# Kernel optimization log

Hardware: AMD Instinct MI355X
Metric: run time of the kernel (lower is better)

## Reference

```python
import jax, jax.numpy as jnp
import numpy as np

B, S, H, DH, DE, DC = 32, 1024, 2, 64, 128, 64  # batch, seq, heads, dim_head, dim_emb, dim_ctx


def setup_inputs() -> dict:
    key = jax.random.key(0)
    ks = jax.random.split(key, 16)
    p = lambda k, shp: (jax.random.normal(k, shp, dtype=jnp.float32) * 0.02)
    return {
        "queries_it": jax.random.normal(ks[0], (B, S, DE), dtype=jnp.float32),
        "queries_ctx": jax.random.normal(ks[1], (B, S, DC), dtype=jnp.float32),
        "keys_it": jax.random.normal(ks[2], (B, S, DE), dtype=jnp.float32),
        "keys_ctx": jax.random.normal(ks[3], (B, S, DC), dtype=jnp.float32),
        "sigma_noise": jax.random.uniform(ks[4], (B, H), dtype=jnp.float32),
        "noise": jax.random.normal(ks[5], (B, 2, S, S), dtype=jnp.float32),
        "Wq_it": p(ks[6], (DH, DE)), "bq_it": jnp.zeros((DH,), jnp.float32),
        "Wk_it": p(ks[7], (DH, DE)), "bk_it": jnp.zeros((DH,), jnp.float32),
        "Wq_ctx": p(ks[8], (DH, DC)), "bq_ctx": jnp.zeros((DH,), jnp.float32),
        "Wk_ctx": p(ks[9], (DH, DC)), "bk_ctx": jnp.zeros((DH,), jnp.float32),
        "Wv": p(ks[10], (DE, DE)), "bv": jnp.zeros((DE,), jnp.float32),
        "W1": p(ks[11], (H, 2)), "b1": jnp.zeros((H,), jnp.float32),
        "W2": p(ks[12], (H, H)), "b2": jnp.zeros((H,), jnp.float32),
    }


def reference(queries_it, queries_ctx, keys_it, keys_ctx, sigma_noise, noise,
              Wq_it, bq_it, Wk_it, bk_it, Wq_ctx, bq_ctx, Wk_ctx, bk_ctx,
              Wv, bv, W1, b1, W2, b2):
    # dual QK projections
    Q_it = queries_it @ Wq_it.T + bq_it          # [B,Sq,DH]
    K_it = keys_it @ Wk_it.T + bk_it             # [B,Sk,DH]
    Q_ctx = queries_ctx @ Wq_ctx.T + bq_ctx
    K_ctx = keys_ctx @ Wk_ctx.T + bk_ctx
    s_it = jnp.einsum('bqd,bkd->bqk', Q_it, K_it)
    s_ctx = jnp.einsum('bqd,bkd->bqk', Q_ctx, K_ctx)
    scores = jnp.stack([s_it, s_ctx], axis=1)    # [B,2,Sq,Sk]
    # additive per-head noise (sigma viewed [B,H,1,1], H==2)
    scores = scores + noise * (sigma_noise[:, :, None, None] ** 2)
    # per-element HDP MLP: 2 -> H -> H over last axis
    x = jnp.transpose(scores, (0, 2, 3, 1))      # [B,Sq,Sk,2]
    h = jax.nn.relu(x @ W1.T + b1)
    s = h @ W2.T + b2                            # [B,Sq,Sk,H]
    s = jnp.transpose(s, (0, 3, 1, 2)) / (DH ** 0.5)  # [B,H,Sq,Sk]
    # key padding mask
    key_mask = jnp.sign(jnp.sum(jnp.abs(keys_it), axis=-1))      # [B,Sk]
    s = jnp.where(key_mask[:, None, None, :] == 0, -1e9, s)
    att = jax.nn.softmax(s, axis=-1)
    # query padding mask (applied after softmax, as in the original)
    query_mask = jnp.sign(jnp.sum(jnp.abs(queries_it), axis=-1))  # [B,Sq]
    att = att * query_mask[:, None, :, None]
    # values
    V = (keys_it @ Wv.T + bv).reshape(B, S, H, DH)               # [B,Sk,H,DH]
    out = jnp.einsum('bhqk,bkhd->bqhd', att, V).reshape(B, S, H * DH)
    return out + queries_it
```

## Files before the change

kernel.cpp:

```cpp
#include <hip/hip_runtime.h>

#define B_N 32
#define S_N 1024

typedef __attribute__((ext_vector_type(8))) short sh8;
typedef __attribute__((ext_vector_type(4))) short sh4;
typedef __attribute__((ext_vector_type(4))) float f4;

#define AS1 __attribute__((address_space(1)))
#define AS3 __attribute__((address_space(3)))

__device__ __forceinline__ short f2bf(float f) {
  unsigned u = __builtin_bit_cast(unsigned, f);
  u += 0x7fff + ((u >> 16) & 1);
  return (short)(u >> 16);
}

#if defined(__has_builtin)
#if __has_builtin(__builtin_amdgcn_mfma_f32_16x16x16bf16_1k)
#define HAVE_MFMA16 1
#endif
#endif
__device__ __forceinline__ f4 mfma16(sh4 a, sh4 b, f4 c) {
#ifdef HAVE_MFMA16
  return __builtin_amdgcn_mfma_f32_16x16x16bf16_1k(a, b, c, 0, 0, 0);
#else
  asm volatile("v_mfma_f32_16x16x16_bf16 %0, %1, %2, %0\n\ts_nop 7\n\ts_nop 7"
               : "+v"(c) : "v"(a), "v"(b));
  return c;
#endif
}

__device__ __forceinline__ sh8 cvt8(const float* src, float& s) {
  f4 x0 = *(const f4*)src;
  f4 x1 = *(const f4*)(src + 4);
  sh8 v;
#pragma unroll
  for (int i = 0; i < 4; ++i) {
    v[i] = f2bf(x0[i]);
    v[4 + i] = f2bf(x1[i]);
    s += fabsf(x0[i]) + fabsf(x1[i]);
  }
  return v;
}

template <int DIN, bool MASK>
__global__ __launch_bounds__(256) void proj_mfma(
    const float* __restrict__ in, const float* __restrict__ W,
    const float* __restrict__ bias, short* __restrict__ out,
    float* __restrict__ mask) {
  constexpr int NSL = DIN / 8;
  constexpr int KT = DIN / 32;
  __shared__ __align__(16) short a_t[128 * DIN];
  __shared__ __align__(16) short w_t[64 * DIN];
  const int tid = threadIdx.x;
  const int wave = tid >> 6, lane = tid & 63;
  const int col = lane & 15, grp = lane >> 4;
  const size_t r0g = (size_t)blockIdx.x * 128;

#pragma unroll
  for (int t = 0; t < 128 * NSL / 256; ++t) {
    const int u = t * 256 + tid, row = u / NSL, sl = u % NSL;
    float s = 0.f;
    sh8 v = cvt8(in + (r0g + row) * DIN + sl * 8, s);
    *(sh8*)&a_t[(row * NSL + (sl ^ (row & (NSL - 1)))) * 8] = v;
    if (MASK) {
      s += __shfl_xor(s, 1); s += __shfl_xor(s, 2);
      s += __shfl_xor(s, 4); s += __shfl_xor(s, 8);
      if ((lane & 15) == 0) mask[r0g + row] = (s != 0.f) ? 1.f : 0.f;
    }
  }
#pragma unroll
  for (int t = 0; t < 64 * NSL / 256; ++t) {
    const int u = t * 256 + tid, row = u / NSL, sl = u % NSL;
    float s = 0.f;
    sh8 v = cvt8(W + (size_t)row * DIN + sl * 8, s);
    *(sh8*)&w_t[(row * NSL + (sl ^ (row & (NSL - 1)))) * 8] = v;
  }
  __syncthreads();

  const int r0 = wave * 32;
  sh8 a[2][KT];
#pragma unroll
  for (int ri = 0; ri < 2; ++ri)
#pragma unroll
    for (int t = 0; t < KT; ++t) {
      const int row = r0 + ri * 16 + col;
      a[ri][t] = *(const sh8*)&a_t[(row * NSL + ((grp + 4 * t) ^ (row & (NSL - 1)))) * 8];
    }
  f4 acc[2][4];
#pragma unroll
  for (int ri = 0; ri < 2; ++ri)
#pragma unroll
    for (int jt = 0; jt < 4; ++jt) acc[ri][jt] = (f4)0.f;
#pragma unroll
  for (int jt = 0; jt < 4; ++jt) {
    const int j = jt * 16 + col;
    sh8 bw[KT];
#pragma unroll
    for (int t = 0; t < KT; ++t)
      bw[t] = *(const sh8*)&w_t[(j * NSL + ((grp + 4 * t) ^ (j & (NSL - 1)))) * 8];
#pragma unroll
    for (int ri = 0; ri < 2; ++ri)
#pragma unroll
      for (int t = 0; t < KT; ++t)
        acc[ri][jt] = __builtin_amdgcn_mfma_f32_16x16x32_bf16(a[ri][t], bw[t], acc[ri][jt], 0, 0, 0);
  }
#pragma unroll
  for (int jt = 0; jt < 4; ++jt) {
    const float bj = bias[jt * 16 + col];
#pragma unroll
    for (int ri = 0; ri < 2; ++ri)
#pragma unroll
      for (int r = 0; r < 4; ++r)
        out[(r0g + r0 + ri * 16 + grp * 4 + r) * 64 + jt * 16 + col] = f2bf(acc[ri][jt][r] + bj);
  }
}

__global__ __launch_bounds__(256) void proj_k_mfma(
    const float* __restrict__ in, const float* __restrict__ Wk, const float* __restrict__ bk_,
    const float* __restrict__ Wv, const float* __restrict__ bv_,
    short* __restrict__ kit, short* __restrict__ vt, float* __restrict__ km) {
  __shared__ __align__(16) char ulds[65536];
  short* a_t = (short*)ulds;
  short* w_t = (short*)(ulds + 32768);
  const int tid = threadIdx.x;
  const int wave = tid >> 6, lane = tid & 63;
  const int col = lane & 15, grp = lane >> 4;
  const size_t r0g = (size_t)blockIdx.x * 128;
  const int bb = (int)(r0g >> 10), s0 = (int)(r0g & 1023);

#pragma unroll
  for (int t = 0; t < 8; ++t) {
    const int u = t * 256 + tid, row = u >> 4, sl = u & 15;
    float s = 0.f;
    sh8 v = cvt8(in + (r0g + row) * 128 + sl * 8, s);
    *(sh8*)&a_t[(row * 16 + (sl ^ (row & 15))) * 8] = v;
    s += __shfl_xor(s, 1); s += __shfl_xor(s, 2);
    s += __shfl_xor(s, 4); s += __shfl_xor(s, 8);
    if ((lane & 15) == 0) km[r0g + row] = (s != 0.f) ? 1.f : 0.f;
  }
#pragma unroll
  for (int t = 0; t < 8; ++t) {
    const int u = t * 256 + tid, row = u >> 4, sl = u & 15;
    const float* src = (row < 64) ? (Wk + (size_t)row * 128) : (Wv + (size_t)(row - 64) * 128);
    float s = 0.f;
    sh8 v = cvt8(src + sl * 8, s);
    *(sh8*)&w_t[(row * 16 + (sl ^ (row & 15))) * 8] = v;
  }
  __syncthreads();

  const int r0 = wave * 32;
  sh8 a[2][4];
#pragma unroll
  for (int ri = 0; ri < 2; ++ri)
#pragma unroll
    for (int t = 0; t < 4; ++t) {
      const int row = r0 + ri * 16 + col;
      a[ri][t] = *(const sh8*)&a_t[(row * 16 + ((grp + 4 * t) ^ (row & 15))) * 8];
    }
  f4 acck[2][4], accv[2][8];
#pragma unroll
  for (int ri = 0; ri < 2; ++ri) {
#pragma unroll
    for (int jt = 0; jt < 4; ++jt) acck[ri][jt] = (f4)0.f;
#pragma unroll
    for (int jt = 0; jt < 8; ++jt) accv[ri][jt] = (f4)0.f;
  }
#pragma unroll
  for (int jt = 0; jt < 8; ++jt) {
    const int j = jt * 16 + col;
    sh8 bw[4];
#pragma unroll
    for (int t = 0; t < 4; ++t)
      bw[t] = *(const sh8*)&w_t[(j * 16 + ((grp + 4 * t) ^ (j & 15))) * 8];
#pragma unroll
    for (int ri = 0; ri < 2; ++ri)
#pragma unroll
      for (int t = 0; t < 4; ++t) {
        f4& dst = (jt < 4) ? acck[ri][jt] : accv[ri][jt - 4];
        dst = __builtin_amdgcn_mfma_f32_16x16x32_bf16(a[ri][t], bw[t], dst, 0, 0, 0);
      }
  }
#pragma unroll
  for (int jt = 0; jt < 4; ++jt) {
    const float bj = bk_[jt * 16 + col];
#pragma unroll
    for (int ri = 0; ri < 2; ++ri)
#pragma unroll
      for (int r = 0; r < 4; ++r)
        kit[(r0g + r0 + ri * 16 + grp * 4 + r) * 64 + jt * 16 + col] = f2bf(acck[ri][jt][r] + bj);
  }
  __syncthreads();
#pragma unroll
  for (int t = 0; t < 4; ++t) {
    const int u = t * 256 + tid, row = u >> 4, sl = u & 15;
    float s = 0.f;
    sh8 v = cvt8(Wv + (size_t)(64 + row) * 128 + sl * 8, s);
    *(sh8*)&w_t[(row * 16 + (sl ^ (row & 15))) * 8] = v;
  }
  __syncthreads();
#pragma unroll
  for (int jt = 0; jt < 4; ++jt) {
    const int j = jt * 16 + col;
    sh8 bw[4];
#pragma unroll
    for (int t = 0; t < 4; ++t)
      bw[t] = *(const sh8*)&w_t[(j * 16 + ((grp + 4 * t) ^ (j & 15))) * 8];
#pragma unroll
    for (int ri = 0; ri < 2; ++ri)
#pragma unroll
      for (int t = 0; t < 4; ++t)
        accv[ri][4 + jt] = __builtin_amdgcn_mfma_f32_16x16x32_bf16(a[ri][t], bw[t], accv[ri][4 + jt], 0, 0, 0);
  }
  __syncthreads();
  short* vtile = (short*)ulds;
#pragma unroll
  for (int vjt = 0; vjt < 8; ++vjt) {
    const int j = vjt * 16 + col;
    const float bvj = bv_[j];
#pragma unroll
    for (int ri = 0; ri < 2; ++ri)
#pragma unroll
      for (int r = 0; r < 4; ++r)
        vtile[j * 136 + r0 + ri * 16 + grp * 4 + r] = f2bf(accv[ri][vjt][r] + bvj);
  }
  __syncthreads();
  const int j2 = tid >> 1, half = tid & 1;
  short* dst = vt + ((size_t)(bb * 128 + j2)) * S_N + s0 + half * 64;
#pragma unroll
  for (int i = 0; i < 8; ++i)
    *(sh8*)(dst + i * 8) = *(const sh8*)&vtile[j2 * 136 + half * 64 + i * 8];
}

__global__ __launch_bounds__(256, 2) void attn_kernel(
    const short* __restrict__ qit, const short* __restrict__ kit,
    const short* __restrict__ qctx, const short* __restrict__ kctx,
    const short* __restrict__ vt,
    const float* __restrict__ noise,
    const float* __restrict__ sigma,
    const float* __restrict__ qmask, const float* __restrict__ kmask,
    const float* __restrict__ qin,
    const float* __restrict__ W1, const float* __restrict__ b1,
    const float* __restrict__ W2, const float* __restrict__ b2,
    float* __restrict__ out) {
  __shared__ __align__(16) char bufs[4][16384];
  __shared__ float kml[1024];
  __shared__ float lsum_lds[4][2][16];

  const int tid = threadIdx.x;
  const int wave = tid >> 6, lane = tid & 63;
  const int bid = blockIdx.x;
  const int wg = ((bid & 7) << 6) | (bid >> 3);
  const int b = wg >> 4, qt = wg & 15;
  const int qblk = qt * 64;
  const int qbase = qblk + wave * 16;
  const int col = lane & 15, grp = lane >> 4;
  const int swk = col & 7;

  const float w100 = W1[0], w101 = W1[1], w110 = W1[2], w111 = W1[3];
  const float bb10 = b1[0], bb11 = b1[1];
  const float sc = 0.125f;
  const float w200 = W2[0] * sc, w201 = W2[1] * sc, w210 = W2[2] * sc, w211 = W2[3] * sc;
  const float bb20 = b2[0] * sc, bb21 = b2[1] * sc;
  float sg0 = sigma[b * 2 + 0]; sg0 *= sg0;
  float sg1 = sigma[b * 2 + 1]; sg1 *= sg1;

  const int qrow = qbase + col;
  sh8 aqit[2], aqctx[2];
#pragma unroll
  for (int t = 0; t < 2; ++t) {
    aqit[t] = *(const sh8*)(qit + ((size_t)(b * S_N + qrow)) * 64 + grp * 8 + t * 32);
    aqctx[t] = *(const sh8*)(qctx + ((size_t)(b * S_N + qrow)) * 64 + grp * 8 + t * 32);
  }

  f4 acc[2][4];
#pragma unroll
  for (int h = 0; h < 2; ++h)
#pragma unroll
    for (int dt = 0; dt < 4; ++dt) acc[h][dt] = (f4)0.f;
  float rs0 = 0.f, rs1 = 0.f;

  const float* nz_g = noise + (size_t)(b * 2) * S_N * S_N;
  const short* kit_g = kit + (size_t)b * S_N * 64;
  const short* kctx_g = kctx + (size_t)b * S_N * 64;
  const short* vt_g = vt + (size_t)b * 128 * S_N;

  for (int i = tid; i < 1024; i += 256) kml[i] = kmask[(size_t)b * S_N + i];

  auto STAGE = [&](char* buf, int kc) {
    if (wave == 0) {
#pragma unroll
      for (int j = 0; j < 2; ++j) {
        const int u = j * 64 + lane, row = u >> 3, sl = u & 7;
        const size_t off = (size_t)(kc + row) * 64 + ((sl ^ (row & 7)) << 3);
        __builtin_amdgcn_global_load_lds((const AS1 unsigned*)(kit_g + off),
                                         (AS3 unsigned*)(buf + j * 1024), 16, 0, 0);
        __builtin_amdgcn_global_load_lds((const AS1 unsigned*)(kctx_g + off),
                                         (AS3 unsigned*)(buf + 2048 + j * 1024), 16, 0, 0);
      }
    } else if (wave == 1) {
#pragma unroll
      for (int j = 0; j < 4; ++j) {
        const int u = j * 64 + lane, d = u >> 1, sl = u & 1;
        const short* g = vt_g + (size_t)d * S_N + kc + ((sl ^ (d & 1)) << 3);
        __builtin_amdgcn_global_load_lds((const AS1 unsigned*)g,
                                         (AS3 unsigned*)(buf + 4096 + j * 1024), 16, 0, 0);
      }
    } else {
#pragma unroll
      for (int j = 0; j < 4; ++j) {
        const int un = (wave - 2) * 4 + j;
        const int u = un * 64 + lane, r = u >> 2, head = r >> 6, q = r & 63, sl = u & 3;
        const float* g = nz_g + (size_t)head * S_N * S_N + (size_t)(qblk + q) * S_N + kc +
                         ((sl ^ (q & 3)) << 2);
        __builtin_amdgcn_global_load_lds((const AS1 unsigned*)g,
                                         (AS3 unsigned*)(buf + 8192 + un * 1024), 16, 0, 0);
      }
    }
  };

  STAGE(bufs[0], 0);
  STAGE(bufs[1], 16);
  STAGE(bufs[2], 32);

#pragma unroll 1
  for (int k = 0; k < 64; ++k) {
    asm volatile("s_waitcnt vmcnt(8)" ::: "memory");
    __builtin_amdgcn_sched_barrier(0);
    __builtin_amdgcn_s_barrier();
    STAGE(bufs[(k + 3) & 3], ((k + 3) & 63) * 16);

    const char* cur = bufs[k & 3];
    const short* Kb = (const short*)cur;
    const short* Cb = (const short*)(cur + 2048);
    const short* Vb = (const short*)(cur + 4096);
    const float* Nb = (const float*)(cur + 8192);

    f4 sit = (f4)0.f, sctx = (f4)0.f;
#pragma unroll
    for (int t = 0; t < 2; ++t) {
      const int so = ((grp + 4 * t) ^ swk) * 8;
      sh8 bk = *(const sh8*)&Kb[col * 64 + so];
      sit = __builtin_amdgcn_mfma_f32_16x16x32_bf16(bk, aqit[t], sit, 0, 0, 0);
      sh8 bc = *(const sh8*)&Cb[col * 64 + so];
      sctx = __builtin_amdgcn_mfma_f32_16x16x32_bf16(bc, aqctx[t], sctx, 0, 0, 0);
    }
    const int qrl = wave * 16 + col;
    const int nso = (grp ^ (col & 3)) << 2;
    f4 n0 = *(const f4*)&Nb[qrl * 16 + nso];
    f4 n1 = *(const f4*)&Nb[(64 + qrl) * 16 + nso];
    f4 km = *(const f4*)&kml[k * 16 + grp * 4];
    sh4 po, pc;
#pragma unroll
    for (int r = 0; r < 4; ++r) {
      float x0 = fmaf(n0[r], sg0, sit[r]);
      float x1 = fmaf(n1[r], sg1, sctx[r]);
      float h0 = fmaxf(fmaf(w101, x1, fmaf(w100, x0, bb10)), 0.f);
      float h1 = fmaxf(fmaf(w111, x1, fmaf(w110, x0, bb11)), 0.f);
      float L0 = fmaf(w201, h1, fmaf(w200, h0, bb20));
      float L1 = fmaf(w211, h1, fmaf(w210, h0, bb21));
      float p0 = __expf(L0) * km[r];
      float p1 = __expf(L1) * km[r];
      rs0 += p0;
      rs1 += p1;
      po[r] = f2bf(p0);
      pc[r] = f2bf(p1);
    }
#pragma unroll
    for (int h = 0; h < 2; ++h) {
      const sh4 pa = h ? pc : po;
#pragma unroll
      for (int dt = 0; dt < 4; ++dt) {
        const int drow = h * 64 + dt * 16 + col;
        const int phys = (grp >> 1) ^ (drow & 1);
        sh4 bv = *(const sh4*)&Vb[drow * 16 + phys * 8 + (grp & 1) * 4];
        acc[h][dt] = mfma16(pa, bv, acc[h][dt]);
      }
    }
  }

  rs0 += __shfl_xor(rs0, 16); rs0 += __shfl_xor(rs0, 32);
  rs1 += __shfl_xor(rs1, 16); rs1 += __shfl_xor(rs1, 32);
  if (lane < 16) {
    lsum_lds[wave][0][col] = rs0;
    lsum_lds[wave][1][col] = rs1;
  }
  __syncthreads();
  f4 ls0 = *(const f4*)&lsum_lds[wave][0][grp * 4];
  f4 ls1 = *(const f4*)&lsum_lds[wave][1][grp * 4];
  f4 qm4 = *(const f4*)(qmask + (size_t)b * S_N + qbase + grp * 4);
#pragma unroll
  for (int h = 0; h < 2; ++h)
#pragma unroll
    for (int dt = 0; dt < 4; ++dt)
#pragma unroll
      for (int r = 0; r < 4; ++r) {
        const float s2 = qm4[r] / (h ? ls1[r] : ls0[r]);
        const size_t o = ((size_t)(b * S_N + qbase + grp * 4 + r)) * 128 + h * 64 + dt * 16 + col;
        out[o] = acc[h][dt][r] * s2 + qin[o];
      }
}

extern "C" void kernel_launch(void* const* d_in, const int* in_sizes, int n_in,
                              void* d_out, int out_size, void* d_ws, size_t ws_size,
                              hipStream_t stream) {
  const float* queries_it = (const float*)d_in[0];
  const float* queries_ctx = (const float*)d_in[1];
  const float* keys_it = (const float*)d_in[2];
  const float* keys_ctx = (const float*)d_in[3];
  const float* sigma = (const float*)d_in[4];
  const float* noise = (const float*)d_in[5];
  const float* Wq_it = (const float*)d_in[6];
  const float* bq_it = (const float*)d_in[7];
  const float* Wk_it = (const float*)d_in[8];
  const float* bk_it = (const float*)d_in[9];
  const float* Wq_ctx = (const float*)d_in[10];
  const float* bq_ctx = (const float*)d_in[11];
  const float* Wk_ctx = (const float*)d_in[12];
  const float* bk_ctx = (const float*)d_in[13];
  const float* Wv = (const float*)d_in[14];
  const float* bv = (const float*)d_in[15];
  const float* W1 = (const float*)d_in[16];
  const float* b1 = (const float*)d_in[17];
  const float* W2 = (const float*)d_in[18];
  const float* b2 = (const float*)d_in[19];
  float* out = (float*)d_out;

  char* ws = (char*)d_ws;
  short* qit = (short*)(ws);
  short* kit = (short*)(ws + (4ull << 20));
  short* qctx = (short*)(ws + (8ull << 20));
  short* kctx = (short*)(ws + (12ull << 20));
  short* vt = (short*)(ws + (16ull << 20));
  float* qmask = (float*)(ws + (24ull << 20));
  float* kmask = (float*)(ws + (24ull << 20) + (size_t)B_N * S_N * 4);

  const int NB = B_N * S_N / 128;
  proj_mfma<128, true><<<dim3(NB), 256, 0, stream>>>(queries_it, Wq_it, bq_it, qit, qmask);
  proj_k_mfma<<<dim3(NB), 256, 0, stream>>>(keys_it, Wk_it, bk_it, Wv, bv, kit, vt, kmask);
  proj_mfma<64, false><<<dim3(NB), 256, 0, stream>>>(queries_ctx, Wq_ctx, bq_ctx, qctx, nullptr);
  proj_mfma<64, false><<<dim3(NB), 256, 0, stream>>>(keys_ctx, Wk_ctx, bk_ctx, kctx, nullptr);

  attn_kernel<<<dim3(B_N * (S_N / 64)), 256, 0, stream>>>(
      qit, kit, qctx, kctx, vt, noise, sigma, qmask, kmask, queries_it,
      W1, b1, W2, b2, out);
}
```

Measured before the change: 127.0 us.

## Shrink attention workgroups to 32 queries with 2 waves and triple buffering

The attention kernel now uses 128-thread workgroups that each handle 32 query rows, so twice as many workgroups are launched. The staging pipeline drops from 4 to 3 LDS buffers of 12 KB, and the K/V/noise loads are redistributed across the two waves. The key mask is stored in LDS as bf16 to save space. The aim is lower LDS use per workgroup and higher occupancy, at the cost of loading each K/V tile twice as often per query row and a shallower prefetch depth.

```diff
diff --git a/kernel.cpp b/kernel.cpp
--- a/kernel.cpp
+++ b/kernel.cpp
@@ -14,6 +14,10 @@
   unsigned u = __builtin_bit_cast(unsigned, f);
   u += 0x7fff + ((u >> 16) & 1);
   return (short)(u >> 16);
+}
+__device__ __forceinline__ float bf2f(short s) {
+  unsigned u = ((unsigned)(unsigned short)s) << 16;
+  return __builtin_bit_cast(float, u);
 }
 
 #if defined(__has_builtin)
@@ -233,7 +237,7 @@
     *(sh8*)(dst + i * 8) = *(const sh8*)&vtile[j2 * 136 + half * 64 + i * 8];
 }
 
-__global__ __launch_bounds__(256, 2) void attn_kernel(
+__global__ __launch_bounds__(128, 2) void attn_kernel(
     const short* __restrict__ qit, const short* __restrict__ kit,
     const short* __restrict__ qctx, const short* __restrict__ kctx,
     const short* __restrict__ vt,
@@ -244,16 +248,16 @@
     const float* __restrict__ W1, const float* __restrict__ b1,
     const float* __restrict__ W2, const float* __restrict__ b2,
     float* __restrict__ out) {
-  __shared__ __align__(16) char bufs[4][16384];
-  __shared__ float kml[1024];
-  __shared__ float lsum_lds[4][2][16];
+  __shared__ __align__(16) char bufs[3][12288];
+  __shared__ unsigned short kml[1024];
+  __shared__ float lsum_lds[2][2][16];
 
   const int tid = threadIdx.x;
   const int wave = tid >> 6, lane = tid & 63;
   const int bid = blockIdx.x;
-  const int wg = ((bid & 7) << 6) | (bid >> 3);
-  const int b = wg >> 4, qt = wg & 15;
-  const int qblk = qt * 64;
+  const int wg = ((bid & 7) << 7) | (bid >> 3);
+  const int b = wg >> 5, qt = wg & 31;
+  const int qblk = qt * 32;
   const int qbase = qblk + wave * 16;
   const int col = lane & 15, grp = lane >> 4;
   const int swk = col & 7;
@@ -286,7 +290,8 @@
   const short* kctx_g = kctx + (size_t)b * S_N * 64;
   const short* vt_g = vt + (size_t)b * 128 * S_N;
 
-  for (int i = tid; i < 1024; i += 256) kml[i] = kmask[(size_t)b * S_N + i];
+  for (int i = tid; i < 1024; i += 128)
+    kml[i] = (unsigned short)f2bf(kmask[(size_t)b * S_N + i]);
 
   auto STAGE = [&](char* buf, int kc) {
     if (wave == 0) {
@@ -299,43 +304,52 @@
         __builtin_amdgcn_global_load_lds((const AS1 unsigned*)(kctx_g + off),
                                          (AS3 unsigned*)(buf + 2048 + j * 1024), 16, 0, 0);
       }
-    } else if (wave == 1) {
-#pragma unroll
-      for (int j = 0; j < 4; ++j) {
-        const int u = j * 64 + lane, d = u >> 1, sl = u & 1;
+#pragma unroll
+      for (int un = 0; un < 2; ++un) {
+        const int u = un * 64 + lane, d = u >> 1, sl = u & 1;
         const short* g = vt_g + (size_t)d * S_N + kc + ((sl ^ (d & 1)) << 3);
         __builtin_amdgcn_global_load_lds((const AS1 unsigned*)g,
-                                         (AS3 unsigned*)(buf + 4096 + j * 1024), 16, 0, 0);
+                                         (AS3 unsigned*)(buf + 4096 + un * 1024), 16, 0, 0);
       }
     } else {
 #pragma unroll
+      for (int un = 2; un < 4; ++un) {
+        const int u = un * 64 + lane, d = u >> 1, sl = u & 1;
+        const short* g = vt_g + (size_t)d * S_N + kc + ((sl ^ (d & 1)) << 3);
+        __builtin_amdgcn_global_load_lds((const AS1 unsigned*)g,
+                                         (AS3 unsigned*)(buf + 4096 + un * 1024), 16, 0, 0);
+      }
+#pragma unroll
       for (int j = 0; j < 4; ++j) {
-        const int un = (wave - 2) * 4 + j;
-        const int u = un * 64 + lane, r = u >> 2, head = r >> 6, q = r & 63, sl = u & 3;
+        const int u = j * 64 + lane, r = u >> 2, head = r >> 5, q = r & 31, sl = u & 3;
         const float* g = nz_g + (size_t)head * S_N * S_N + (size_t)(qblk + q) * S_N + kc +
-                         ((sl ^ (q & 3)) << 2);
+                         ((sl ^ (r & 3)) << 2);
         __builtin_amdgcn_global_load_lds((const AS1 unsigned*)g,
-                                         (AS3 unsigned*)(buf + 8192 + un * 1024), 16, 0, 0);
+                                         (AS3 unsigned*)(buf + 8192 + j * 1024), 16, 0, 0);
       }
     }
   };
 
   STAGE(bufs[0], 0);
   STAGE(bufs[1], 16);
-  STAGE(bufs[2], 32);
-
+
+  int cur = 0;
 #pragma unroll 1
   for (int k = 0; k < 64; ++k) {
-    asm volatile("s_waitcnt vmcnt(8)" ::: "memory");
+    asm volatile("s_waitcnt vmcnt(6)" ::: "memory");
     __builtin_amdgcn_sched_barrier(0);
     __builtin_amdgcn_s_barrier();
-    STAGE(bufs[(k + 3) & 3], ((k + 3) & 63) * 16);
-
-    const char* cur = bufs[k & 3];
-    const short* Kb = (const short*)cur;
-    const short* Cb = (const short*)(cur + 2048);
-    const short* Vb = (const short*)(cur + 4096);
-    const float* Nb = (const float*)(cur + 8192);
+    {
+      int nb = cur + 2;
+      if (nb >= 3) nb -= 3;
+      STAGE(bufs[nb], ((k + 2) & 63) * 16);
+    }
+
+    const char* cb = bufs[cur];
+    const short* Kb = (const short*)cb;
+    const short* Cb = (const short*)(cb + 2048);
+    const short* Vb = (const short*)(cb + 4096);
+    const float* Nb = (const float*)(cb + 8192);
 
     f4 sit = (f4)0.f, sctx = (f4)0.f;
 #pragma unroll
@@ -349,8 +363,8 @@
     const int qrl = wave * 16 + col;
     const int nso = (grp ^ (col & 3)) << 2;
     f4 n0 = *(const f4*)&Nb[qrl * 16 + nso];
-    f4 n1 = *(const f4*)&Nb[(64 + qrl) * 16 + nso];
-    f4 km = *(const f4*)&kml[k * 16 + grp * 4];
+    f4 n1 = *(const f4*)&Nb[(32 + qrl) * 16 + nso];
+    sh4 kmv = *(const sh4*)&kml[k * 16 + grp * 4];
     sh4 po, pc;
 #pragma unroll
     for (int r = 0; r < 4; ++r) {
@@ -360,8 +374,9 @@
       float h1 = fmaxf(fmaf(w111, x1, fmaf(w110, x0, bb11)), 0.f);
       float L0 = fmaf(w201, h1, fmaf(w200, h0, bb20));
       float L1 = fmaf(w211, h1, fmaf(w210, h0, bb21));
-      float p0 = __expf(L0) * km[r];
-      float p1 = __expf(L1) * km[r];
+      const float kmf = bf2f(kmv[r]);
+      float p0 = __expf(L0) * kmf;
+      float p1 = __expf(L1) * kmf;
       rs0 += p0;
       rs1 += p1;
       po[r] = f2bf(p0);
@@ -378,6 +393,8 @@
         acc[h][dt] = mfma16(pa, bv, acc[h][dt]);
       }
     }
+    ++cur;
+    if (cur >= 3) cur = 0;
   }
 
   rs0 += __shfl_xor(rs0, 16); rs0 += __shfl_xor(rs0, 32);
@@ -442,7 +459,7 @@
   proj_mfma<64, false><<<dim3(NB), 256, 0, stream>>>(queries_ctx, Wq_ctx, bq_ctx, qctx, nullptr);
   proj_mfma<64, false><<<dim3(NB), 256, 0, stream>>>(keys_ctx, Wk_ctx, bk_ctx, kctx, nullptr);
 
-  attn_kernel<<<dim3(B_N * (S_N / 64)), 256, 0, stream>>>(
+  attn_kernel<<<dim3(B_N * (S_N / 32)), 128, 0, stream>>>(
       qit, kit, qctx, kctx, vt, noise, sigma, qmask, kmask, queries_it,
       W1, b1, W2, b2, out);
 }
```

Result: slower. 151.0 us (+18.9%).

## Rebalance attention staging loads across waves and merge ctx projection launches

Applied to the files above, without the earlier changes.

Each wave now loads its own slice of the noise tile, and the K/ctx/V loads are split evenly across waves instead of one wave carrying the whole noise load. A second, finer vmcnt wait lets the QK MFMAs start before each wave's noise data has landed. The two ctx projection kernels are merged into one launch, cutting launch overhead and the tail between them. A __syncthreads is added after filling the key mask in LDS, which fixes a potential race at a small sync cost.

```diff
diff --git a/kernel.cpp b/kernel.cpp
--- a/kernel.cpp
+++ b/kernel.cpp
@@ -45,10 +45,10 @@
 }
 
 template <int DIN, bool MASK>
-__global__ __launch_bounds__(256) void proj_mfma(
+__device__ __forceinline__ void dev_proj(
     const float* __restrict__ in, const float* __restrict__ W,
     const float* __restrict__ bias, short* __restrict__ out,
-    float* __restrict__ mask) {
+    float* __restrict__ mask, int blk) {
   constexpr int NSL = DIN / 8;
   constexpr int KT = DIN / 32;
   __shared__ __align__(16) short a_t[128 * DIN];
@@ -56,7 +56,7 @@
   const int tid = threadIdx.x;
   const int wave = tid >> 6, lane = tid & 63;
   const int col = lane & 15, grp = lane >> 4;
-  const size_t r0g = (size_t)blockIdx.x * 128;
+  const size_t r0g = (size_t)blk * 128;
 
 #pragma unroll
   for (int t = 0; t < 128 * NSL / 256; ++t) {
@@ -115,6 +115,24 @@
       for (int r = 0; r < 4; ++r)
         out[(r0g + r0 + ri * 16 + grp * 4 + r) * 64 + jt * 16 + col] = f2bf(acc[ri][jt][r] + bj);
   }
+}
+
+__global__ __launch_bounds__(256) void proj_q_kernel(
+    const float* __restrict__ in, const float* __restrict__ W,
+    const float* __restrict__ bias, short* __restrict__ out,
+    float* __restrict__ mask) {
+  dev_proj<128, true>(in, W, bias, out, mask, blockIdx.x);
+}
+
+__global__ __launch_bounds__(256) void proj_ctx2_kernel(
+    const float* __restrict__ in0, const float* __restrict__ W0,
+    const float* __restrict__ b0, short* __restrict__ o0,
+    const float* __restrict__ in1, const float* __restrict__ W1_,
+    const float* __restrict__ b1_, short* __restrict__ o1, int nb) {
+  const int sel = blockIdx.x >= nb;
+  const int blk = sel ? (blockIdx.x - nb) : blockIdx.x;
+  dev_proj<64, false>(sel ? in1 : in0, sel ? W1_ : W0, sel ? b1_ : b0,
+                      sel ? o1 : o0, nullptr, blk);
 }
 
 __global__ __launch_bounds__(256) void proj_k_mfma(
@@ -287,6 +305,7 @@
   const short* vt_g = vt + (size_t)b * 128 * S_N;
 
   for (int i = tid; i < 1024; i += 256) kml[i] = kmask[(size_t)b * S_N + i];
+  __syncthreads();
 
   auto STAGE = [&](char* buf, int kc) {
     if (wave == 0) {
@@ -296,27 +315,31 @@
         const size_t off = (size_t)(kc + row) * 64 + ((sl ^ (row & 7)) << 3);
         __builtin_amdgcn_global_load_lds((const AS1 unsigned*)(kit_g + off),
                                          (AS3 unsigned*)(buf + j * 1024), 16, 0, 0);
+      }
+    } else if (wave == 1) {
+#pragma unroll
+      for (int j = 0; j < 2; ++j) {
+        const int u = j * 64 + lane, row = u >> 3, sl = u & 7;
+        const size_t off = (size_t)(kc + row) * 64 + ((sl ^ (row & 7)) << 3);
         __builtin_amdgcn_global_load_lds((const AS1 unsigned*)(kctx_g + off),
                                          (AS3 unsigned*)(buf + 2048 + j * 1024), 16, 0, 0);
       }
-    } else if (wave == 1) {
-#pragma unroll
-      for (int j = 0; j < 4; ++j) {
-        const int u = j * 64 + lane, d = u >> 1, sl = u & 1;
+    } else {
+#pragma unroll
+      for (int i = 0; i < 2; ++i) {
+        const int un = (wave - 2) * 2 + i;
+        const int u = un * 64 + lane, d = u >> 1, sl = u & 1;
         const short* g = vt_g + (size_t)d * S_N + kc + ((sl ^ (d & 1)) << 3);
         __builtin_amdgcn_global_load_lds((const AS1 unsigned*)g,
-                                         (AS3 unsigned*)(buf + 4096 + j * 1024), 16, 0, 0);
-      }
-    } else {
-#pragma unroll
-      for (int j = 0; j < 4; ++j) {
-        const int un = (wave - 2) * 4 + j;
-        const int u = un * 64 + lane, r = u >> 2, head = r >> 6, q = r & 63, sl = u & 3;
-        const float* g = nz_g + (size_t)head * S_N * S_N + (size_t)(qblk + q) * S_N + kc +
-                         ((sl ^ (q & 3)) << 2);
-        __builtin_amdgcn_global_load_lds((const AS1 unsigned*)g,
-                                         (AS3 unsigned*)(buf + 8192 + un * 1024), 16, 0, 0);
-      }
+                                         (AS3 unsigned*)(buf + 4096 + un * 1024), 16, 0, 0);
+      }
+    }
+#pragma unroll
+    for (int h = 0; h < 2; ++h) {
+      const int q = lane >> 2, sg = lane & 3, jq = sg ^ (q & 3);
+      const float* g = nz_g + (size_t)h * S_N * S_N + (size_t)(qbase + q) * S_N + kc + jq * 4;
+      __builtin_amdgcn_global_load_lds((const AS1 unsigned*)g,
+                                       (AS3 unsigned*)(buf + 8192 + wave * 2048 + h * 1024), 16, 0, 0);
     }
   };
 
@@ -326,7 +349,7 @@
 
 #pragma unroll 1
   for (int k = 0; k < 64; ++k) {
-    asm volatile("s_waitcnt vmcnt(8)" ::: "memory");
+    asm volatile("s_waitcnt vmcnt(10)" ::: "memory");
     __builtin_amdgcn_sched_barrier(0);
     __builtin_amdgcn_s_barrier();
     STAGE(bufs[(k + 3) & 3], ((k + 3) & 63) * 16);
@@ -335,7 +358,6 @@
     const short* Kb = (const short*)cur;
     const short* Cb = (const short*)(cur + 2048);
     const short* Vb = (const short*)(cur + 4096);
-    const float* Nb = (const float*)(cur + 8192);
 
     f4 sit = (f4)0.f, sctx = (f4)0.f;
 #pragma unroll
@@ -346,10 +368,12 @@
       sh8 bc = *(const sh8*)&Cb[col * 64 + so];
       sctx = __builtin_amdgcn_mfma_f32_16x16x32_bf16(bc, aqctx[t], sctx, 0, 0, 0);
     }
-    const int qrl = wave * 16 + col;
-    const int nso = (grp ^ (col & 3)) << 2;
-    f4 n0 = *(const f4*)&Nb[qrl * 16 + nso];
-    f4 n1 = *(const f4*)&Nb[(64 + qrl) * 16 + nso];
+    asm volatile("s_waitcnt vmcnt(12)" ::: "memory");
+    __builtin_amdgcn_sched_barrier(0);
+    const float* Nw = (const float*)(cur + 8192 + wave * 2048);
+    const int jq = grp ^ (col & 3);
+    f4 n0 = *(const f4*)&Nw[col * 16 + jq * 4];
+    f4 n1 = *(const f4*)&Nw[256 + col * 16 + jq * 4];
     f4 km = *(const f4*)&kml[k * 16 + grp * 4];
     sh4 po, pc;
 #pragma unroll
@@ -437,10 +461,10 @@
   float* kmask = (float*)(ws + (24ull << 20) + (size_t)B_N * S_N * 4);
 
   const int NB = B_N * S_N / 128;
-  proj_mfma<128, true><<<dim3(NB), 256, 0, stream>>>(queries_it, Wq_it, bq_it, qit, qmask);
+  proj_q_kernel<<<dim3(NB), 256, 0, stream>>>(queries_it, Wq_it, bq_it, qit, qmask);
   proj_k_mfma<<<dim3(NB), 256, 0, stream>>>(keys_it, Wk_it, bk_it, Wv, bv, kit, vt, kmask);
-  proj_mfma<64, false><<<dim3(NB), 256, 0, stream>>>(queries_ctx, Wq_ctx, bq_ctx, qctx, nullptr);
-  proj_mfma<64, false><<<dim3(NB), 256, 0, stream>>>(keys_ctx, Wk_ctx, bk_ctx, kctx, nullptr);
+  proj_ctx2_kernel<<<dim3(2 * NB), 256, 0, stream>>>(
+      queries_ctx, Wq_ctx, bq_ctx, qctx, keys_ctx, Wk_ctx, bk_ctx, kctx, NB);
 
   attn_kernel<<<dim3(B_N * (S_N / 64)), 256, 0, stream>>>(
       qit, kit, qctx, kctx, vt, noise, sigma, qmask, kmask, queries_it,
```

After: 131.3 us. +3.4%, slower.
